# Optimization experiments

Measured on AMD Instinct MI355X. Metric: run time of the kernel, lower is better.

Reference implementation:

```python
import jax, jax.numpy as jnp
import numpy as np

N_EMBD = 1024
N_HEAD = 16
HEAD_DIM = N_EMBD // N_HEAD


def setup_inputs() -> dict:
    key = jax.random.key(0)
    k1, k2, k3, k4, k5 = jax.random.split(key, 5)
    B, T, C = 4, 2048, N_EMBD
    s = 1.0 / np.sqrt(C)
    return {
        "x": jax.random.normal(k1, (B, T, C), dtype=jnp.float32),
        "W_attn": jax.random.normal(k2, (C, 3 * C), dtype=jnp.float32) * s,
        "b_attn": jnp.zeros((3 * C,), dtype=jnp.float32),
        "W_proj": jax.random.normal(k3, (C, C), dtype=jnp.float32) * s,
        "b_proj": jnp.zeros((C,), dtype=jnp.float32),
    }


def reference(x, W_attn, b_attn, W_proj, b_proj):
    B, T, C = x.shape
    H, D = N_HEAD, HEAD_DIM
    # fused QKV projection
    qkv = x @ W_attn + b_attn                       # [B,T,3C]
    q, k, v = jnp.split(qkv, 3, axis=2)
    q = q.reshape(B, T, H, D).transpose(0, 2, 1, 3)  # [B,H,T,D]
    k = k.reshape(B, T, H, D).transpose(0, 2, 1, 3)
    v = v.reshape(B, T, H, D).transpose(0, 2, 1, 3)
    # causal scaled dot-product attention
    scale = 1.0 / jnp.sqrt(jnp.asarray(D, dtype=x.dtype))
    scores = jnp.einsum('bhqd,bhkd->bhqk', q, k) * scale  # [B,H,T,T]
    causal = jnp.tril(jnp.ones((T, T), dtype=bool))
    scores = jnp.where(causal[None, None], scores, jnp.finfo(x.dtype).min)
    attn = jax.nn.softmax(scores, axis=-1)
    y = jnp.einsum('bhqk,bhkd->bhqd', attn, v)      # [B,H,T,D]
    y = y.transpose(0, 2, 1, 3).reshape(B, T, C)
    return y @ W_proj + b_proj
```

## Files before the change

kernel.cpp:

```cpp
#include <hip/hip_runtime.h>
#include <hip/hip_bf16.h>
#include <cstdint>

#define B_ 4
#define T_ 2048
#define C_ 1024
#define H_ 16
#define D_ 64
#define M_ (B_*T_)
#define N3 (3*C_)

typedef __bf16 bf16;
typedef __bf16 bf16x8 __attribute__((ext_vector_type(8)));
typedef __bf16 bf16x4 __attribute__((ext_vector_type(4)));
typedef float  floatx4 __attribute__((ext_vector_type(4)));

__device__ __forceinline__ void gl_lds16(const bf16* g, bf16* l) {
  __builtin_amdgcn_global_load_lds(
      (__attribute__((address_space(1))) void*)(void*)g,
      (__attribute__((address_space(3))) void*)(void*)l,
      16, 0, 0);
}

__global__ void cast_to_bf16(const float* __restrict__ in, bf16* __restrict__ out, int n) {
  int i = (blockIdx.x * blockDim.x + threadIdx.x) * 4;
  if (i < n) {
    const float4 f = *(const float4*)(in + i);
    bf16x4 o;
    o.x = (bf16)f.x; o.y = (bf16)f.y; o.z = (bf16)f.z; o.w = (bf16)f.w;
    *(bf16x4*)(out + i) = o;
  }
}

__global__ void transpose_cast(const float* __restrict__ in, bf16* __restrict__ out,
                               int R, int C) {
  __shared__ float tile[32][33];
  int r0 = blockIdx.y * 32, c0 = blockIdx.x * 32;
  int tx = threadIdx.x & 31, ty = threadIdx.x >> 5;
  #pragma unroll
  for (int j = 0; j < 32; j += 8)
    tile[ty + j][tx] = in[(size_t)(r0 + ty + j) * C + c0 + tx];
  __syncthreads();
  #pragma unroll
  for (int j = 0; j < 32; j += 8)
    out[(size_t)(c0 + ty + j) * R + r0 + tx] = (bf16)tile[tx][ty + j];
}

__global__ __launch_bounds__(256)
void transpose_v(const bf16* __restrict__ in, bf16* __restrict__ out) {
  __shared__ __attribute__((aligned(16))) bf16 tileN[64 * 64];
  const int tid = threadIdx.x;
  const int bh = blockIdx.z;
  const int t0 = blockIdx.x * 64;
  const int sk = tid >> 2, scc = tid & 3;
  {
    const bf16* p = in + ((size_t)bh * T_ + t0 + sk) * D_ + scc * 16;
    const bf16x8 r0 = *(const bf16x8*)p;
    const bf16x8 r1 = *(const bf16x8*)(p + 8);
    *(bf16x8*)(tileN + sk * 64 + ((2 * scc)     ^ (sk & 7)) * 8) = r0;
    *(bf16x8*)(tileN + sk * 64 + ((2 * scc + 1) ^ (sk & 7)) * 8) = r1;
  }
  __syncthreads();
  const int tc = (tid & 7) * 8;
  #pragma unroll
  for (int half = 0; half < 2; half++) {
    const int d = (tid >> 3) + half * 32;
    bf16x8 o;
    #pragma unroll
    for (int j = 0; j < 8; j++) {
      const int slot = tc + j;
      const int row = (slot & 3) + 4 * ((slot >> 3) & 3) + 16 * ((slot >> 2) & 1)
                    + 32 * (slot >> 5);
      o[j] = tileN[row * 64 + (((d >> 3) ^ (row & 7)) * 8) + (d & 7)];
    }
    *(bf16x8*)(out + ((size_t)bh * D_ + d) * T_ + t0 + tc) = o;
  }
}

template<int MODE>
__global__ __launch_bounds__(256)
void gemm_bt(const bf16* __restrict__ A, const bf16* __restrict__ Bt,
             const float* __restrict__ bias, float* __restrict__ out,
             bf16* __restrict__ qo, bf16* __restrict__ ko, bf16* __restrict__ vo,
             int M, int N, int K)
{
  __shared__ __attribute__((aligned(16))) bf16 As[128 * 32];
  __shared__ __attribute__((aligned(16))) bf16 Bs[128 * 32];

  const int tid  = threadIdx.x;
  const int w    = tid >> 6;
  const int lane = tid & 63;
  const int quad = lane >> 4;
  const int l16  = lane & 15;
  const int wm   = w & 1, wn = w >> 1;
  const int m0   = blockIdx.y * 128, n0 = blockIdx.x * 128;

  floatx4 acc[4][4] = {};

  const int lrow = lane >> 2;
  const int lk   = (lane & 3) * 8;

  const bf16* aptr = A  + (size_t)(m0 + w * 32 + lrow) * K + lk;
  const bf16* bptr = Bt + (size_t)(n0 + w * 32 + lrow) * K + lk;
  bf16* asl = As + w * 1024;
  bf16* bsl = Bs + w * 1024;

  for (int k0 = 0; k0 < K; k0 += 32) {
    gl_lds16(aptr,          asl);
    gl_lds16(aptr + 16 * K, asl + 512);
    gl_lds16(bptr,          bsl);
    gl_lds16(bptr + 16 * K, bsl + 512);
    aptr += 32; bptr += 32;
    __syncthreads();

    bf16x8 af[4], bfb[4];
    #pragma unroll
    for (int i = 0; i < 4; i++)
      af[i] = *(const bf16x8*)(As + (wm * 64 + i * 16 + l16) * 32 + quad * 8);
    #pragma unroll
    for (int i = 0; i < 4; i++)
      bfb[i] = *(const bf16x8*)(Bs + (wn * 64 + i * 16 + l16) * 32 + quad * 8);
    #pragma unroll
    for (int mi = 0; mi < 4; mi++)
      #pragma unroll
      for (int ni = 0; ni < 4; ni++)
        acc[mi][ni] = __builtin_amdgcn_mfma_f32_16x16x32_bf16(af[mi], bfb[ni], acc[mi][ni], 0, 0, 0);
    __syncthreads();
  }

  #pragma unroll
  for (int mi = 0; mi < 4; mi++) {
    #pragma unroll
    for (int ni = 0; ni < 4; ni++) {
      const int col = n0 + wn * 64 + ni * 16 + l16;
      const float bv = bias[col];
      #pragma unroll
      for (int r = 0; r < 4; r++) {
        const int row = m0 + wm * 64 + mi * 16 + quad * 4 + r;
        const float val = acc[mi][ni][r] + bv;
        if (MODE == 0) {
          const int b = row >> 11, t = row & 2047;
          const int s = col >> 10, c = col & 1023;
          const int h = c >> 6,  d = c & 63;
          bf16* dst = (s == 0) ? qo : (s == 1) ? ko : vo;
          dst[((size_t)(b * H_ + h) * T_ + t) * D_ + d] = (bf16)val;
        } else {
          out[(size_t)row * N + col] = val;
        }
      }
    }
  }
}

__device__ __forceinline__ void stage8(const bf16* g, int K, bf16* lds, int lane) {
  const int r = lane >> 3, s = (lane & 7) ^ r;
  gl_lds16(g + (size_t)r * K + s * 8, lds);
}
__device__ __forceinline__ void stage_half(const bf16* g, int K, bf16* lds, int wv, int lane) {
  stage8(g + (size_t)(wv * 16) * K,     K, lds + (wv * 16) * 64, lane);
  stage8(g + (size_t)(wv * 16 + 8) * K, K, lds + (wv * 16 + 8) * 64, lane);
}

#define GBAR  __builtin_amdgcn_s_barrier()
#define WLGKM do { asm volatile("s_waitcnt lgkmcnt(0)"); __builtin_amdgcn_sched_barrier(0); } while (0)
#define WVM4  do { asm volatile("s_waitcnt vmcnt(4)");   __builtin_amdgcn_sched_barrier(0); } while (0)

template<int MODE>
__global__ __launch_bounds__(512, 2)
void gemm256(const bf16* __restrict__ A, const bf16* __restrict__ Bt,
             const float* __restrict__ bias, float* __restrict__ out,
             bf16* __restrict__ qo, bf16* __restrict__ ko, bf16* __restrict__ vo,
             int M, int N, int K)
{
  __shared__ __attribute__((aligned(16))) bf16 As[2][256 * 64];
  __shared__ __attribute__((aligned(16))) bf16 Bs[2][256 * 64];

  const int tid  = threadIdx.x;
  const int wv   = tid >> 6, lane = tid & 63;
  const int quad = lane >> 4, l16 = lane & 15;
  const int wm   = wv >> 2, wn = wv & 3;
  const int NTT  = K >> 6;

  const int nbx = gridDim.x;
  const int nwg = nbx * gridDim.y;
  const int bid = blockIdx.y * nbx + blockIdx.x;
  const int cpx = nwg >> 3;
  const int swz = (bid & 7) * cpx + (bid >> 3);
  const int n0  = (swz % nbx) * 256, m0 = (swz / nbx) * 256;

  floatx4 acc[8][4] = {};

  const bf16* Abase = A  + (size_t)m0 * K;
  const bf16* Bbase = Bt + (size_t)n0 * K;

  stage_half(Abase,                  K, As[0],            wv, lane);
  stage_half(Abase + (size_t)128*K,  K, As[0] + 128 * 64, wv, lane);
  stage_half(Bbase,                  K, Bs[0],            wv, lane);
  stage_half(Bbase + (size_t)128*K,  K, Bs[0] + 128 * 64, wv, lane);
  stage_half(Bbase + 64,             K, Bs[1],            wv, lane);
  stage_half(Abase + 64,             K, As[1],            wv, lane);
  WVM4;
  GBAR;

#define LOADA(qm)                                                          \
  _Pragma("unroll")                                                        \
  for (int mi = 0; mi < 4; mi++) {                                         \
    const int row = wm * 128 + (qm) * 64 + mi * 16 + l16;                  \
    const bf16* rp = bufA + row * 64;                                      \
    af[mi][0] = *(const bf16x8*)(rp + (( quad      ^ (row & 7)) * 8));     \
    af[mi][1] = *(const bf16x8*)(rp + (((4 | quad) ^ (row & 7)) * 8));     \
  }
#define LOADB(qn)                                                          \
  _Pragma("unroll")                                                        \
  for (int ni = 0; ni < 2; ni++) {                                         \
    const int row = wn * 64 + (qn) * 32 + ni * 16 + l16;                   \
    const bf16* rp = bufB + row * 64;                                      \
    bfr[(qn)*2+ni][0] = *(const bf16x8*)(rp + (( quad      ^ (row & 7)) * 8)); \
    bfr[(qn)*2+ni][1] = *(const bf16x8*)(rp + (((4 | quad) ^ (row & 7)) * 8)); \
  }
#define MM(qm, qn)                                                         \
  __builtin_amdgcn_s_setprio(1);                                           \
  _Pragma("unroll")                                                        \
  for (int mi = 0; mi < 4; mi++)                                           \
    _Pragma("unroll")                                                      \
    for (int ni = 0; ni < 2; ni++) {                                       \
      acc[(qm)*4+mi][(qn)*2+ni] = __builtin_amdgcn_mfma_f32_16x16x32_bf16( \
          af[mi][0], bfr[(qn)*2+ni][0], acc[(qm)*4+mi][(qn)*2+ni], 0, 0, 0); \
      acc[(qm)*4+mi][(qn)*2+ni] = __builtin_amdgcn_mfma_f32_16x16x32_bf16( \
          af[mi][1], bfr[(qn)*2+ni][1], acc[(qm)*4+mi][(qn)*2+ni], 0, 0, 0); \
    }                                                                      \
  __builtin_amdgcn_s_setprio(0);

  #pragma unroll 1
  for (int t = 0; t < NTT; t++) {
    const int cur = t & 1;
    const bf16* bufA = As[cur];
    const bf16* bufB = Bs[cur];
    bf16* nA = As[cur ^ 1];
    bf16* nB = Bs[cur ^ 1];
    bf16* cA = As[cur];
    bf16* cB = Bs[cur];
    const int kn1 = (t + 1) * 64, kn2 = (t + 2) * 64;
    const bool h1 = (t + 1 < NTT), h2 = (t + 2 < NTT);

    bf16x8 af[4][2], bfr[4][2];

    LOADA(0);
    LOADB(0);
    if (h1) stage_half(Abase + (size_t)128 * K + kn1, K, nA + 128 * 64, wv, lane);
    GBAR;
    WLGKM;
    MM(0, 0);
    GBAR;

    LOADB(1);
    if (h1) stage_half(Bbase + (size_t)128 * K + kn1, K, nB + 128 * 64, wv, lane);
    GBAR;
    WLGKM;
    MM(0, 1);
    GBAR;

    LOADA(1);
    if (h2) stage_half(Bbase + kn2, K, cB, wv, lane);
    GBAR;
    WLGKM;
    MM(1, 0);
    GBAR;

    if (h2) stage_half(Abase + kn2, K, cA, wv, lane);
    GBAR;
    MM(1, 1);
    WVM4;
    GBAR;
  }

#undef LOADA
#undef LOADB
#undef MM

  #pragma unroll
  for (int mi8 = 0; mi8 < 8; mi8++) {
    #pragma unroll
    for (int nf = 0; nf < 4; nf++) {
      const int col = n0 + wn * 64 + nf * 16 + l16;
      const float bv = bias[col];
      #pragma unroll
      for (int r = 0; r < 4; r++) {
        const int row = m0 + wm * 128 + mi8 * 16 + quad * 4 + r;
        const float val = acc[mi8][nf][r] + bv;
        if (MODE == 0) {
          const int b = row >> 11, tt = row & 2047;
          const int s = col >> 10, c = col & 1023;
          const int h = c >> 6, d = c & 63;
          bf16* dst = (s == 0) ? qo : (s == 1) ? ko : vo;
          dst[((size_t)(b * H_ + h) * T_ + tt) * D_ + d] = (bf16)val;
        } else {
          out[(size_t)row * N + col] = val;
        }
      }
    }
  }
}

__global__ __launch_bounds__(256)
void attn_kernel(const bf16* __restrict__ Q, const bf16* __restrict__ Kp,
                 const bf16* __restrict__ Vtp, bf16* __restrict__ Y)
{
  __shared__ __attribute__((aligned(16))) bf16 Ks[2][64 * 72];
  __shared__ __attribute__((aligned(16))) bf16 Vs[2][64 * 72];

  const int tid  = threadIdx.x;
  const int w    = tid >> 6, lane = tid & 63;
  const int quad = lane >> 4, l16 = lane & 15;
  const int bh = blockIdx.x;
  const int b = bh >> 4, h = bh & 15;

  const int sk = tid >> 2;
  const int sc = (tid & 3) * 16;

  const float SC = 0.125f * 1.44269504088896f;

  const int qt = 15 - (int)blockIdx.y;
  const int q0 = qt * 128;
  const int nch = 2 * qt + 2;

  bf16x8 qf[2][2];
  #pragma unroll
  for (int mt = 0; mt < 2; mt++) {
    const bf16* qp = Q + ((size_t)bh * T_ + q0 + mt * 64 + w * 16 + l16) * D_ + quad * 8;
    qf[mt][0] = *(const bf16x8*)qp;
    qf[mt][1] = *(const bf16x8*)(qp + 32);
  }

  floatx4 o[2][4] = {};
  float l_r[2] = {0.f, 0.f};

  const bf16* kpp = Kp  + (size_t)bh * T_ * D_ + (size_t)sk * D_ + sc;
  const bf16* vpp = Vtp + (size_t)bh * D_ * T_ + (size_t)sk * T_ + sc;

  {
    const bf16x8 k0 = *(const bf16x8*)kpp, k1 = *(const bf16x8*)(kpp + 8);
    const bf16x8 v0 = *(const bf16x8*)vpp, v1 = *(const bf16x8*)(vpp + 8);
    bf16* kd = Ks[0] + sk * 72 + sc;
    *(bf16x8*)kd = k0; *(bf16x8*)(kd + 8) = k1;
    bf16* vd = Vs[0] + sk * 72 + sc;
    *(bf16x8*)vd = v0; *(bf16x8*)(vd + 8) = v1;
    kpp += 64 * D_; vpp += 64;
  }
  __syncthreads();

  #pragma unroll 1
  for (int c = 0; c < nch; c++) {
    const int cur = c & 1;

    bf16x8 nk0, nk1, nv0, nv1;
    const bool have = (c + 1 < nch);
    if (have) {
      nk0 = *(const bf16x8*)kpp; nk1 = *(const bf16x8*)(kpp + 8);
      nv0 = *(const bf16x8*)vpp; nv1 = *(const bf16x8*)(vpp + 8);
      kpp += 64 * D_; vpp += 64;
    }

    const bf16* KsC = Ks[cur];
    const bf16* VsC = Vs[cur];
    const int kv0 = c * 64;
    const bool act0 = (c < nch - 1);

    floatx4 s[2][4];
    __builtin_amdgcn_s_setprio(1);
    #pragma unroll
    for (int nt = 0; nt < 4; nt++) {
      const bf16x8 kf0 = *(const bf16x8*)(KsC + (nt * 16 + l16) * 72 + quad * 8);
      const bf16x8 kf1 = *(const bf16x8*)(KsC + (nt * 16 + l16) * 72 + 32 + quad * 8);
      if (act0) {
        floatx4 z = {};
        z = __builtin_amdgcn_mfma_f32_16x16x32_bf16(kf0, qf[0][0], z, 0, 0, 0);
        s[0][nt] = __builtin_amdgcn_mfma_f32_16x16x32_bf16(kf1, qf[0][1], z, 0, 0, 0);
      }
      floatx4 z = {};
      z = __builtin_amdgcn_mfma_f32_16x16x32_bf16(kf0, qf[1][0], z, 0, 0, 0);
      s[1][nt] = __builtin_amdgcn_mfma_f32_16x16x32_bf16(kf1, qf[1][1], z, 0, 0, 0);
    }
    __builtin_amdgcn_s_setprio(0);

    bf16x8 vfr[4][2];
    #pragma unroll
    for (int nt = 0; nt < 4; nt++) {
      vfr[nt][0] = *(const bf16x8*)(VsC + (nt * 16 + l16) * 72 + quad * 8);
      vfr[nt][1] = *(const bf16x8*)(VsC + (nt * 16 + l16) * 72 + 32 + quad * 8);
    }

    #pragma unroll
    for (int mt = 0; mt < 2; mt++) {
      if (mt == 0 && !act0) continue;
      const bool diag = (c == 2 * qt + mt);
      const int qrow = q0 + mt * 64 + w * 16 + l16;
      float e[4][4];
      float ls0 = 0.f, ls1 = 0.f;
      #pragma unroll
      for (int nt = 0; nt < 4; nt++) {
        #pragma unroll
        for (int r = 0; r < 4; r++) {
          float x = s[mt][nt][r];
          if (diag) {
            if (kv0 + nt * 16 + quad * 4 + r > qrow) x = -1e30f;
          }
          const float ev = __builtin_amdgcn_exp2f(fmaf(x, SC, -8.f));
          e[nt][r] = ev;
          if (nt & 1) ls1 += ev; else ls0 += ev;
        }
      }
      l_r[mt] += ls0 + ls1;

      union { uint32_t u[4]; bf16x8 v; } pa0, pa1;
      #pragma unroll
      for (int jj = 0; jj < 4; jj++) {
        pa0.u[jj] = __builtin_amdgcn_perm(
            __float_as_uint(e[(jj >> 1)][(jj & 1) * 2 + 1]),
            __float_as_uint(e[(jj >> 1)][(jj & 1) * 2]), 0x07060302u);
        pa1.u[jj] = __builtin_amdgcn_perm(
            __float_as_uint(e[2 + (jj >> 1)][(jj & 1) * 2 + 1]),
            __float_as_uint(e[2 + (jj >> 1)][(jj & 1) * 2]), 0x07060302u);
      }
      __builtin_amdgcn_s_setprio(1);
      #pragma unroll
      for (int nt = 0; nt < 4; nt++) {
        o[mt][nt] = __builtin_amdgcn_mfma_f32_16x16x32_bf16(pa0.v, vfr[nt][0], o[mt][nt], 0, 0, 0);
        o[mt][nt] = __builtin_amdgcn_mfma_f32_16x16x32_bf16(pa1.v, vfr[nt][1], o[mt][nt], 0, 0, 0);
      }
      __builtin_amdgcn_s_setprio(0);
    }

    if (have) {
      bf16* kd = Ks[cur ^ 1] + sk * 72 + sc;
      *(bf16x8*)kd = nk0; *(bf16x8*)(kd + 8) = nk1;
      bf16* vd = Vs[cur ^ 1] + sk * 72 + sc;
      *(bf16x8*)vd = nv0; *(bf16x8*)(vd + 8) = nv1;
    }
    __syncthreads();
  }

  #pragma unroll
  for (int mt = 0; mt < 2; mt++) {
    float ls = l_r[mt];
    ls += __shfl_xor(ls, 16);
    ls += __shfl_xor(ls, 32);
    const float invls = 1.f / ls;
    #pragma unroll
    for (int r = 0; r < 4; r++) {
      const float inv = __shfl(invls, (lane & 48) + quad * 4 + r);
      const int t = q0 + mt * 64 + w * 16 + quad * 4 + r;
      #pragma unroll
      for (int nt = 0; nt < 4; nt++)
        Y[((size_t)b * T_ + t) * C_ + h * D_ + nt * 16 + l16] = (bf16)(o[mt][nt][r] * inv);
    }
  }
}

extern "C" void kernel_launch(void* const* d_in, const int* in_sizes, int n_in,
                              void* d_out, int out_size, void* d_ws, size_t ws_size,
                              hipStream_t stream)
{
  const float* x      = (const float*)d_in[0];
  const float* W_attn = (const float*)d_in[1];
  const float* b_attn = (const float*)d_in[2];
  const float* W_proj = (const float*)d_in[3];
  const float* b_proj = (const float*)d_in[4];
  float* out = (float*)d_out;

  bf16* xb  = (bf16*)d_ws;
  bf16* wat = xb  + (size_t)M_ * C_;
  bf16* wpt = wat + (size_t)N3 * C_;
  bf16* qb  = wpt + (size_t)C_ * C_;
  bf16* kb  = qb  + (size_t)M_ * C_;
  bf16* vb  = kb  + (size_t)M_ * C_;
  bf16* yb  = vb  + (size_t)M_ * C_;
  bf16* vtb = xb;

  cast_to_bf16<<<dim3(M_ * C_ / 1024), 256, 0, stream>>>(x, xb, M_ * C_);
  transpose_cast<<<dim3(N3 / 32, C_ / 32), 256, 0, stream>>>(W_attn, wat, C_, N3);
  transpose_cast<<<dim3(C_ / 32, C_ / 32), 256, 0, stream>>>(W_proj, wpt, C_, C_);
  gemm256<0><<<dim3(N3 / 256, M_ / 256), 512, 0, stream>>>(
      xb, wat, b_attn, nullptr, qb, kb, vb, M_, N3, C_);
  transpose_v<<<dim3(T_ / 64, 1, B_ * H_), 256, 0, stream>>>(vb, vtb);
  attn_kernel<<<dim3(B_ * H_, 16), 256, 0, stream>>>(qb, kb, vtb, yb);
  gemm_bt<1><<<dim3(C_ / 128, M_ / 128), 256, 0, stream>>>(
      yb, wpt, b_proj, out, nullptr, nullptr, nullptr, M_, C_, C_);
}
```

Measured before the change: 270.1 us.

## Shrink QKV GEMM tile to 256x128 with a two-phase staging pipeline

The QKV projection GEMM moves from 256x256 tiles to 256x128 tiles, which halves the B shared-memory buffer and the per-wave accumulators. The grid doubles to 768 workgroups, giving better occupancy and tail balance across the CUs. The k-loop is rebuilt from four MFMA phases into two, each with its own staging of the next A/B quarters and adjusted vmcnt waits. The cost is less data reuse per tile, so more global and LDS traffic is spent per FLOP.

```diff
diff --git a/kernel.cpp b/kernel.cpp
--- a/kernel.cpp
+++ b/kernel.cpp
@@ -152,28 +152,27 @@
   }
 }
 
+
 __device__ __forceinline__ void stage8(const bf16* g, int K, bf16* lds, int lane) {
   const int r = lane >> 3, s = (lane & 7) ^ r;
   gl_lds16(g + (size_t)r * K + s * 8, lds);
 }
-__device__ __forceinline__ void stage_half(const bf16* g, int K, bf16* lds, int wv, int lane) {
-  stage8(g + (size_t)(wv * 16) * K,     K, lds + (wv * 16) * 64, lane);
-  stage8(g + (size_t)(wv * 16 + 8) * K, K, lds + (wv * 16 + 8) * 64, lane);
+__device__ __forceinline__ void stage_q(const bf16* g, int K, bf16* lds, int wv, int lane) {
+  stage8(g + (size_t)(wv * 8) * K, K, lds + (wv * 8) * 64, lane);
 }
 
 #define GBAR  __builtin_amdgcn_s_barrier()
 #define WLGKM do { asm volatile("s_waitcnt lgkmcnt(0)"); __builtin_amdgcn_sched_barrier(0); } while (0)
-#define WVM4  do { asm volatile("s_waitcnt vmcnt(4)");   __builtin_amdgcn_sched_barrier(0); } while (0)
-
-template<int MODE>
+#define WVM2  do { asm volatile("s_waitcnt vmcnt(2)");   __builtin_amdgcn_sched_barrier(0); } while (0)
+
 __global__ __launch_bounds__(512, 2)
-void gemm256(const bf16* __restrict__ A, const bf16* __restrict__ Bt,
-             const float* __restrict__ bias, float* __restrict__ out,
-             bf16* __restrict__ qo, bf16* __restrict__ ko, bf16* __restrict__ vo,
-             int M, int N, int K)
+void gemm_qkv(const bf16* __restrict__ A, const bf16* __restrict__ Bt,
+              const float* __restrict__ bias,
+              bf16* __restrict__ qo, bf16* __restrict__ ko, bf16* __restrict__ vo,
+              int M, int N, int K)
 {
   __shared__ __attribute__((aligned(16))) bf16 As[2][256 * 64];
-  __shared__ __attribute__((aligned(16))) bf16 Bs[2][256 * 64];
+  __shared__ __attribute__((aligned(16))) bf16 Bs[2][128 * 64];
 
   const int tid  = threadIdx.x;
   const int wv   = tid >> 6, lane = tid & 63;
@@ -182,52 +181,53 @@
   const int NTT  = K >> 6;
 
   const int nbx = gridDim.x;
-  const int nwg = nbx * gridDim.y;
   const int bid = blockIdx.y * nbx + blockIdx.x;
-  const int cpx = nwg >> 3;
+  const int cpx = (nbx * gridDim.y) >> 3;
   const int swz = (bid & 7) * cpx + (bid >> 3);
-  const int n0  = (swz % nbx) * 256, m0 = (swz / nbx) * 256;
-
-  floatx4 acc[8][4] = {};
+  const int n0  = (swz % nbx) * 128, m0 = (swz / nbx) * 256;
+
+  floatx4 acc[8][2] = {};
 
   const bf16* Abase = A  + (size_t)m0 * K;
   const bf16* Bbase = Bt + (size_t)n0 * K;
 
-  stage_half(Abase,                  K, As[0],            wv, lane);
-  stage_half(Abase + (size_t)128*K,  K, As[0] + 128 * 64, wv, lane);
-  stage_half(Bbase,                  K, Bs[0],            wv, lane);
-  stage_half(Bbase + (size_t)128*K,  K, Bs[0] + 128 * 64, wv, lane);
-  stage_half(Bbase + 64,             K, Bs[1],            wv, lane);
-  stage_half(Abase + 64,             K, As[1],            wv, lane);
-  WVM4;
+  stage_q(Abase,                    K, As[0],            wv, lane);
+  stage_q(Abase + (size_t)128*K,    K, As[0] + 128 * 64, wv, lane);
+  stage_q(Abase + (size_t) 64*K,    K, As[0] +  64 * 64, wv, lane);
+  stage_q(Abase + (size_t)192*K,    K, As[0] + 192 * 64, wv, lane);
+  stage_q(Bbase,                    K, Bs[0],            wv, lane);
+  stage_q(Bbase + (size_t) 64*K,    K, Bs[0] +  64 * 64, wv, lane);
+  stage_q(Abase + 64,               K, As[1],            wv, lane);
+  stage_q(Abase + (size_t)128*K+64, K, As[1] + 128 * 64, wv, lane);
+  WVM2;
   GBAR;
 
-#define LOADA(qm)                                                          \
+#define LOADA(ph)                                                          \
   _Pragma("unroll")                                                        \
   for (int mi = 0; mi < 4; mi++) {                                         \
-    const int row = wm * 128 + (qm) * 64 + mi * 16 + l16;                  \
+    const int row = wm * 128 + (ph) * 64 + mi * 16 + l16;                  \
     const bf16* rp = bufA + row * 64;                                      \
     af[mi][0] = *(const bf16x8*)(rp + (( quad      ^ (row & 7)) * 8));     \
     af[mi][1] = *(const bf16x8*)(rp + (((4 | quad) ^ (row & 7)) * 8));     \
   }
-#define LOADB(qn)                                                          \
+#define LOADB                                                              \
   _Pragma("unroll")                                                        \
   for (int ni = 0; ni < 2; ni++) {                                         \
-    const int row = wn * 64 + (qn) * 32 + ni * 16 + l16;                   \
+    const int row = wn * 32 + ni * 16 + l16;                               \
     const bf16* rp = bufB + row * 64;                                      \
-    bfr[(qn)*2+ni][0] = *(const bf16x8*)(rp + (( quad      ^ (row & 7)) * 8)); \
-    bfr[(qn)*2+ni][1] = *(const bf16x8*)(rp + (((4 | quad) ^ (row & 7)) * 8)); \
-  }
-#define MM(qm, qn)                                                         \
+    bfr[ni][0] = *(const bf16x8*)(rp + (( quad      ^ (row & 7)) * 8));    \
+    bfr[ni][1] = *(const bf16x8*)(rp + (((4 | quad) ^ (row & 7)) * 8));    \
+  }
+#define MM(ph)                                                             \
   __builtin_amdgcn_s_setprio(1);                                           \
   _Pragma("unroll")                                                        \
   for (int mi = 0; mi < 4; mi++)                                           \
     _Pragma("unroll")                                                      \
     for (int ni = 0; ni < 2; ni++) {                                       \
-      acc[(qm)*4+mi][(qn)*2+ni] = __builtin_amdgcn_mfma_f32_16x16x32_bf16( \
-          af[mi][0], bfr[(qn)*2+ni][0], acc[(qm)*4+mi][(qn)*2+ni], 0, 0, 0); \
-      acc[(qm)*4+mi][(qn)*2+ni] = __builtin_amdgcn_mfma_f32_16x16x32_bf16( \
-          af[mi][1], bfr[(qn)*2+ni][1], acc[(qm)*4+mi][(qn)*2+ni], 0, 0, 0); \
+      acc[(ph)*4+mi][ni] = __builtin_amdgcn_mfma_f32_16x16x32_bf16(        \
+          af[mi][0], bfr[ni][0], acc[(ph)*4+mi][ni], 0, 0, 0);             \
+      acc[(ph)*4+mi][ni] = __builtin_amdgcn_mfma_f32_16x16x32_bf16(        \
+          af[mi][1], bfr[ni][1], acc[(ph)*4+mi][ni], 0, 0, 0);             \
     }                                                                      \
   __builtin_amdgcn_s_setprio(0);
 
@@ -239,38 +239,33 @@
     bf16* nA = As[cur ^ 1];
     bf16* nB = Bs[cur ^ 1];
     bf16* cA = As[cur];
-    bf16* cB = Bs[cur];
     const int kn1 = (t + 1) * 64, kn2 = (t + 2) * 64;
     const bool h1 = (t + 1 < NTT), h2 = (t + 2 < NTT);
 
-    bf16x8 af[4][2], bfr[4][2];
+    bf16x8 af[4][2], bfr[2][2];
 
     LOADA(0);
-    LOADB(0);
-    if (h1) stage_half(Abase + (size_t)128 * K + kn1, K, nA + 128 * 64, wv, lane);
+    LOADB;
+    if (h1) {
+      stage_q(Abase + (size_t) 64*K + kn1, K, nA +  64 * 64, wv, lane);
+      stage_q(Abase + (size_t)192*K + kn1, K, nA + 192 * 64, wv, lane);
+      stage_q(Bbase + kn1,                 K, nB,            wv, lane);
+      stage_q(Bbase + (size_t) 64*K + kn1, K, nB +  64 * 64, wv, lane);
+    }
     GBAR;
     WLGKM;
-    MM(0, 0);
+    MM(0);
     GBAR;
 
-    LOADB(1);
-    if (h1) stage_half(Bbase + (size_t)128 * K + kn1, K, nB + 128 * 64, wv, lane);
+    LOADA(1);
+    if (h2) {
+      stage_q(Abase + kn2,                 K, cA,            wv, lane);
+      stage_q(Abase + (size_t)128*K + kn2, K, cA + 128 * 64, wv, lane);
+    }
     GBAR;
     WLGKM;
-    MM(0, 1);
-    GBAR;
-
-    LOADA(1);
-    if (h2) stage_half(Bbase + kn2, K, cB, wv, lane);
-    GBAR;
-    WLGKM;
-    MM(1, 0);
-    GBAR;
-
-    if (h2) stage_half(Abase + kn2, K, cA, wv, lane);
-    GBAR;
-    MM(1, 1);
-    WVM4;
+    MM(1);
+    WVM2;
     GBAR;
   }
 
@@ -281,22 +276,18 @@
   #pragma unroll
   for (int mi8 = 0; mi8 < 8; mi8++) {
     #pragma unroll
-    for (int nf = 0; nf < 4; nf++) {
-      const int col = n0 + wn * 64 + nf * 16 + l16;
+    for (int nf = 0; nf < 2; nf++) {
+      const int col = n0 + wn * 32 + nf * 16 + l16;
       const float bv = bias[col];
       #pragma unroll
       for (int r = 0; r < 4; r++) {
         const int row = m0 + wm * 128 + mi8 * 16 + quad * 4 + r;
         const float val = acc[mi8][nf][r] + bv;
-        if (MODE == 0) {
-          const int b = row >> 11, tt = row & 2047;
-          const int s = col >> 10, c = col & 1023;
-          const int h = c >> 6, d = c & 63;
-          bf16* dst = (s == 0) ? qo : (s == 1) ? ko : vo;
-          dst[((size_t)(b * H_ + h) * T_ + tt) * D_ + d] = (bf16)val;
-        } else {
-          out[(size_t)row * N + col] = val;
-        }
+        const int b = row >> 11, tt = row & 2047;
+        const int s = col >> 10, c = col & 1023;
+        const int h = c >> 6, d = c & 63;
+        bf16* dst = (s == 0) ? qo : (s == 1) ? ko : vo;
+        dst[((size_t)(b * H_ + h) * T_ + tt) * D_ + d] = (bf16)val;
       }
     }
   }
@@ -480,8 +471,8 @@
   cast_to_bf16<<<dim3(M_ * C_ / 1024), 256, 0, stream>>>(x, xb, M_ * C_);
   transpose_cast<<<dim3(N3 / 32, C_ / 32), 256, 0, stream>>>(W_attn, wat, C_, N3);
   transpose_cast<<<dim3(C_ / 32, C_ / 32), 256, 0, stream>>>(W_proj, wpt, C_, C_);
-  gemm256<0><<<dim3(N3 / 256, M_ / 256), 512, 0, stream>>>(
-      xb, wat, b_attn, nullptr, qb, kb, vb, M_, N3, C_);
+  gemm_qkv<<<dim3(N3 / 128, M_ / 256), 512, 0, stream>>>(
+      xb, wat, b_attn, qb, kb, vb, M_, N3, C_);
   transpose_v<<<dim3(T_ / 64, 1, B_ * H_), 256, 0, stream>>>(vb, vtb);
   attn_kernel<<<dim3(B_ * H_, 16), 256, 0, stream>>>(qb, kb, vtb, yb);
   gemm_bt<1><<<dim3(C_ / 128, M_ / 128), 256, 0, stream>>>(
```

Result: no change. 267.1 us (-1.1%).
